# Kernel optimization log

Measured on AMD Instinct MI355X. Metric: run time of the kernel, lower is better.

The kernel has to match this reference:

```python
import jax, jax.numpy as jnp
import numpy as np


def _w1_1d(u, v):
    """POT-style 1D Wasserstein-1 between empirical dists of u and v (uniform weights).

    u, v: (N,) sample values. Follows ot.wasserstein_1d: sort samples, build
    cumulative weights, merge quantile levels, evaluate both quantile functions
    via searchsorted, and integrate |Q_u - Q_v| dq.
    """
    n = u.shape[0]
    u_s = jnp.sort(u)
    v_s = jnp.sort(v)
    # uniform weights -> identical cumulative weights for both distributions
    cw = jnp.cumsum(jnp.full((n,), 1.0 / n, dtype=u.dtype))
    qs = jnp.sort(jnp.concatenate([cw, cw]))  # (2N,) merged quantile levels
    idx = jnp.clip(jnp.searchsorted(cw, qs), 0, n - 1)  # quantile-function lookup
    uq = u_s[idx]
    vq = v_s[idx]
    delta = jnp.diff(qs, prepend=jnp.zeros((1,), dtype=u.dtype))  # dq segments
    return jnp.sum(delta * jnp.abs(uq - vq))


def setup_inputs() -> dict:
    key = jax.random.key(0)
    k1, k2 = jax.random.split(key)
    B, N = 4096, 4096
    return {
        "spectra_predict": jax.random.uniform(k1, (B, N), dtype=jnp.float32),
        "spectra_true": jax.random.uniform(k2, (B, N), dtype=jnp.float32),
    }


def reference(spectra_predict, spectra_true):
    # Original: wasserstein_1d(pred.T, true.T) batches over columns (= rows of
    # the untransposed [B, N] tensors), then mean over the batch.
    losses = jax.vmap(_w1_1d)(spectra_predict, spectra_true)  # (B,)
    return jnp.mean(losses)
```

## Files before the change

### kernel.cpp

```cpp
#include <hip/hip_runtime.h>


constexpr int N_ELEM  = 4096;
constexpr int V       = 32;
constexpr int THREADS = 256;

__device__ __forceinline__ float ce2(float x, float o, bool keep_min) {
    return ((o < x) != keep_min) ? x : o;
}

template<int S>
__device__ __forceinline__ void reg_merge(float r[V]) {
    #pragma unroll
    for (int k = 0; k < V; ++k) {
        if ((k & (S >> 1)) == 0) {
            const int j = k ^ (S - 1);
            const float a = r[k], b = r[j];
            r[k] = fminf(a, b);
            r[j] = fmaxf(a, b);
        }
    }
    #pragma unroll
    for (int s = S >> 2; s >= 1; s >>= 1) {
        #pragma unroll
        for (int k = 0; k < V; ++k) {
            if ((k & s) == 0) {
                const float a = r[k], b = r[k + s];
                r[k]     = fminf(a, b);
                r[k + s] = fmaxf(a, b);
            }
        }
    }
}

__device__ __forceinline__ void reg_tail_asc(float r[V]) {
    #pragma unroll
    for (int s = 16; s >= 1; s >>= 1) {
        #pragma unroll
        for (int k = 0; k < V; ++k) {
            if ((k & s) == 0) {
                const float a = r[k], b = r[k + s];
                r[k]     = fminf(a, b);
                r[k + s] = fmaxf(a, b);
            }
        }
    }
}

template<int CTRL>
__device__ __forceinline__ float dpp_x(float x) {
    return __int_as_float(__builtin_amdgcn_mov_dpp(__float_as_int(x), CTRL, 0xF, 0xF, true));
}
__device__ __forceinline__ float bperm_x(int pa, float x) {
    return __int_as_float(__builtin_amdgcn_ds_bpermute(pa, __float_as_int(x)));
}

template<int M>
__device__ __forceinline__ void xor_pass(float ru[V], float rv[V], int lane) {
    const bool keep_min = (lane & M) == 0;
    if constexpr (M == 1 || M == 2 || M == 8) {
        constexpr int ctrl = (M == 1) ? 0xB1 : (M == 2) ? 0x4E : 0x128;
        #pragma unroll
        for (int k = 0; k < V; ++k) {
            ru[k] = ce2(ru[k], dpp_x<ctrl>(ru[k]), keep_min);
            rv[k] = ce2(rv[k], dpp_x<ctrl>(rv[k]), keep_min);
        }
    } else {
        const int pa = (lane ^ M) << 2;
        float tu[16], tv[16];
        #pragma unroll
        for (int k = 0; k < 16; ++k) tu[k] = bperm_x(pa, ru[k]);
        #pragma unroll
        for (int k = 0; k < 16; ++k) tv[k] = bperm_x(pa, rv[k]);
        #pragma unroll
        for (int k = 0; k < 16; ++k) ru[k] = ce2(ru[k], tu[k], keep_min);
        #pragma unroll
        for (int k = 0; k < 16; ++k) tu[k] = bperm_x(pa, ru[16 + k]);
        #pragma unroll
        for (int k = 0; k < 16; ++k) rv[k] = ce2(rv[k], tv[k], keep_min);
        #pragma unroll
        for (int k = 0; k < 16; ++k) tv[k] = bperm_x(pa, rv[16 + k]);
        #pragma unroll
        for (int k = 0; k < 16; ++k) ru[16 + k] = ce2(ru[16 + k], tu[k], keep_min);
        #pragma unroll
        for (int k = 0; k < 16; ++k) rv[16 + k] = ce2(rv[16 + k], tv[k], keep_min);
    }
}

template<int MMAX>
__device__ __forceinline__ void cross_descend(float ru[V], float rv[V], int lane) {
    if constexpr (MMAX >= 32) xor_pass<32>(ru, rv, lane);
    if constexpr (MMAX >= 16) xor_pass<16>(ru, rv, lane);
    if constexpr (MMAX >= 8)  xor_pass<8>(ru, rv, lane);
    if constexpr (MMAX >= 4)  xor_pass<4>(ru, rv, lane);
    if constexpr (MMAX >= 2)  xor_pass<2>(ru, rv, lane);
    if constexpr (MMAX >= 1)  xor_pass<1>(ru, rv, lane);
    reg_tail_asc(ru);
    reg_tail_asc(rv);
}

template<int X>
static constexpr int mirror_dpp_ctrl() {
    return X == 1 ? 0xB1 : X == 3 ? 0x1B : X == 7 ? 0x141 : X == 15 ? 0x140 : -1;
}

template<int X>
__device__ __forceinline__ void mirror_pass(float ru[V], float rv[V], int lane) {
    const bool keep_min = (lane & ((X + 1) >> 1)) == 0;
    constexpr int ctrl = mirror_dpp_ctrl<X>();
    if constexpr (ctrl != -1) {
        #pragma unroll
        for (int k = 0; k < V / 2; ++k) {
            const int j = V - 1 - k;
            const float ua = dpp_x<ctrl>(ru[j]);
            const float ub = dpp_x<ctrl>(ru[k]);
            ru[k] = ce2(ru[k], ua, keep_min);
            ru[j] = ce2(ru[j], ub, keep_min);
            const float va = dpp_x<ctrl>(rv[j]);
            const float vb = dpp_x<ctrl>(rv[k]);
            rv[k] = ce2(rv[k], va, keep_min);
            rv[j] = ce2(rv[j], vb, keep_min);
        }
    } else {
        const int pa = (lane ^ X) << 2;
        #pragma unroll
        for (int k = 0; k < V / 2; ++k) {
            const int j = V - 1 - k;
            const float ua = bperm_x(pa, ru[j]);
            const float ub = bperm_x(pa, ru[k]);
            ru[k] = ce2(ru[k], ua, keep_min);
            ru[j] = ce2(ru[j], ub, keep_min);
            const float va = bperm_x(pa, rv[j]);
            const float vb = bperm_x(pa, rv[k]);
            rv[k] = ce2(rv[k], va, keep_min);
            rv[j] = ce2(rv[j], vb, keep_min);
        }
    }
}

template<int S>
__device__ __forceinline__ void stage_m(float ru[V], float rv[V], int lane) {
    mirror_pass<(S >> 5) - 1>(ru, rv, lane);
    cross_descend<(S >> 7)>(ru, rv, lane);
}

__global__ __launch_bounds__(THREADS, 4) void w1_rows_kernel(
    const float* __restrict__ pred,
    const float* __restrict__ tru,
    float* __restrict__ out,
    float scale)
{
    __shared__ float xbuf[2 * 128 * 33];
    __shared__ float wsum[THREADS / 64];

    const int tid  = threadIdx.x;
    const int t    = tid & 127;
    const int lane = tid & 63;
    const int row  = blockIdx.x * 2 + (tid >> 7);
    const size_t base = (size_t)row * N_ELEM + (size_t)t * V;

    float ru[V], rv[V];
    {
        const float4* u4 = (const float4*)(pred + base);
        const float4* v4 = (const float4*)(tru  + base);
        #pragma unroll
        for (int c = 0; c < V / 4; ++c) {
            float4 a = u4[c], b = v4[c];
            ru[4*c+0] = a.x; ru[4*c+1] = a.y; ru[4*c+2] = a.z; ru[4*c+3] = a.w;
            rv[4*c+0] = b.x; rv[4*c+1] = b.y; rv[4*c+2] = b.z; rv[4*c+3] = b.w;
        }
    }

    reg_merge<2>(ru);  reg_merge<2>(rv);
    reg_merge<4>(ru);  reg_merge<4>(rv);
    reg_merge<8>(ru);  reg_merge<8>(rv);
    reg_merge<16>(ru); reg_merge<16>(rv);
    reg_merge<32>(ru); reg_merge<32>(rv);

    stage_m<64>(ru, rv, lane);
    stage_m<128>(ru, rv, lane);
    stage_m<256>(ru, rv, lane);
    stage_m<512>(ru, rv, lane);
    stage_m<1024>(ru, rv, lane);
    stage_m<2048>(ru, rv, lane);

    {
        const bool is_upper = (t & 64) != 0;
        const int  slot_row = (tid >> 7) * 64;
        const int  my_u = (slot_row + lane) * 33;
        const int  my_v = 4224 + my_u;
        const int  pa_u = (slot_row + (63 - lane)) * 33;
        const int  pa_v = 4224 + pa_u;

        if (is_upper) {
            #pragma unroll
            for (int k = 0; k < V; ++k) xbuf[my_u + k] = ru[k];
            #pragma unroll
            for (int k = 0; k < V; ++k) xbuf[my_v + k] = rv[k];
        }
        __syncthreads();
        if (!is_upper) {
            #pragma unroll
            for (int k = 0; k < V; ++k) {
                const int  e = V - 1 - k;
                const float ou = xbuf[pa_u + e];
                const float ov = xbuf[pa_v + e];
                const float mu = fmaxf(ru[k], ou);
                const float mv = fmaxf(rv[k], ov);
                ru[k] = fminf(ru[k], ou);
                rv[k] = fminf(rv[k], ov);
                xbuf[pa_u + e] = mu;
                xbuf[pa_v + e] = mv;
            }
        }
        __syncthreads();
        if (is_upper) {
            #pragma unroll
            for (int k = 0; k < V; ++k) ru[k] = xbuf[my_u + k];
            #pragma unroll
            for (int k = 0; k < V; ++k) rv[k] = xbuf[my_v + k];
        }

        cross_descend<32>(ru, rv, lane);
    }

    float part = 0.f;
    #pragma unroll
    for (int k = 0; k < V; ++k) part += fabsf(ru[k] - rv[k]);

    #pragma unroll
    for (int off = 32; off > 0; off >>= 1)
        part += __shfl_down(part, off, 64);

    const int wid = tid >> 6;
    if (lane == 0) wsum[wid] = part;
    __syncthreads();
    if (tid == 0) {
        float tot = wsum[0] + wsum[1] + wsum[2] + wsum[3];
        atomicAdd(out, tot * scale);
    }
}

extern "C" void kernel_launch(void* const* d_in, const int* in_sizes, int n_in,
                              void* d_out, int out_size, void* d_ws, size_t ws_size,
                              hipStream_t stream)
{
    (void)n_in; (void)out_size; (void)d_ws; (void)ws_size;

    const float* pred = (const float*)d_in[0];
    const float* tru  = (const float*)d_in[1];
    float* out = (float*)d_out;

    const int B = in_sizes[0] / N_ELEM;

    hipMemsetAsync(out, 0, sizeof(float), stream);

    const float scale = 1.0f / ((float)N_ELEM * (float)B);
    w1_rows_kernel<<<B / 2, THREADS, 0, stream>>>(pred, tru, out, scale);
}
```

Measured before the change: 240.8 us.

## Split pred and true sorting across separate thread groups with 512-thread blocks

```diff
diff --git a/kernel.cpp b/kernel.cpp
--- a/kernel.cpp
+++ b/kernel.cpp
@@ -3,7 +3,7 @@
 
 constexpr int N_ELEM  = 4096;
 constexpr int V       = 32;
-constexpr int THREADS = 256;
+constexpr int THREADS = 512;
 
 __device__ __forceinline__ float ce2(float x, float o, bool keep_min) {
     return ((o < x) != keep_min) ? x : o;
@@ -56,47 +56,38 @@
 }
 
 template<int M>
-__device__ __forceinline__ void xor_pass(float ru[V], float rv[V], int lane) {
+__device__ __forceinline__ void xor_pass1(float r[V], int lane) {
     const bool keep_min = (lane & M) == 0;
     if constexpr (M == 1 || M == 2 || M == 8) {
         constexpr int ctrl = (M == 1) ? 0xB1 : (M == 2) ? 0x4E : 0x128;
         #pragma unroll
-        for (int k = 0; k < V; ++k) {
-            ru[k] = ce2(ru[k], dpp_x<ctrl>(ru[k]), keep_min);
-            rv[k] = ce2(rv[k], dpp_x<ctrl>(rv[k]), keep_min);
-        }
+        for (int k = 0; k < V; ++k)
+            r[k] = ce2(r[k], dpp_x<ctrl>(r[k]), keep_min);
     } else {
         const int pa = (lane ^ M) << 2;
-        float tu[16], tv[16];
-        #pragma unroll
-        for (int k = 0; k < 16; ++k) tu[k] = bperm_x(pa, ru[k]);
-        #pragma unroll
-        for (int k = 0; k < 16; ++k) tv[k] = bperm_x(pa, rv[k]);
-        #pragma unroll
-        for (int k = 0; k < 16; ++k) ru[k] = ce2(ru[k], tu[k], keep_min);
-        #pragma unroll
-        for (int k = 0; k < 16; ++k) tu[k] = bperm_x(pa, ru[16 + k]);
-        #pragma unroll
-        for (int k = 0; k < 16; ++k) rv[k] = ce2(rv[k], tv[k], keep_min);
-        #pragma unroll
-        for (int k = 0; k < 16; ++k) tv[k] = bperm_x(pa, rv[16 + k]);
-        #pragma unroll
-        for (int k = 0; k < 16; ++k) ru[16 + k] = ce2(ru[16 + k], tu[k], keep_min);
-        #pragma unroll
-        for (int k = 0; k < 16; ++k) rv[16 + k] = ce2(rv[16 + k], tv[k], keep_min);
+        float tt[16];
+        #pragma unroll
+        for (int k = 0; k < 16; ++k) tt[k] = bperm_x(pa, r[k]);
+        #pragma unroll
+        for (int k = 0; k < 16; ++k) {
+            r[k] = ce2(r[k], tt[k], keep_min);
+            tt[k] = bperm_x(pa, r[16 + k]);
+        }
+        #pragma unroll
+        for (int k = 0; k < 16; ++k)
+            r[16 + k] = ce2(r[16 + k], tt[k], keep_min);
     }
 }
 
 template<int MMAX>
-__device__ __forceinline__ void cross_descend(float ru[V], float rv[V], int lane) {
-    if constexpr (MMAX >= 32) xor_pass<32>(ru, rv, lane);
-    if constexpr (MMAX >= 16) xor_pass<16>(ru, rv, lane);
-    if constexpr (MMAX >= 8)  xor_pass<8>(ru, rv, lane);
-    if constexpr (MMAX >= 4)  xor_pass<4>(ru, rv, lane);
-    if constexpr (MMAX >= 2)  xor_pass<2>(ru, rv, lane);
-    if constexpr (MMAX >= 1)  xor_pass<1>(ru, rv, lane);
-    reg_tail_asc(ru);
-    reg_tail_asc(rv);
+__device__ __forceinline__ void cross_descend1(float r[V], int lane) {
+    if constexpr (MMAX >= 32) xor_pass1<32>(r, lane);
+    if constexpr (MMAX >= 16) xor_pass1<16>(r, lane);
+    if constexpr (MMAX >= 8)  xor_pass1<8>(r, lane);
+    if constexpr (MMAX >= 4)  xor_pass1<4>(r, lane);
+    if constexpr (MMAX >= 2)  xor_pass1<2>(r, lane);
+    if constexpr (MMAX >= 1)  xor_pass1<1>(r, lane);
+    reg_tail_asc(r);
 }
 
 template<int X>
@@ -105,128 +96,121 @@
 }
 
 template<int X>
-__device__ __forceinline__ void mirror_pass(float ru[V], float rv[V], int lane) {
+__device__ __forceinline__ void mirror_pass1(float r[V], int lane) {
     const bool keep_min = (lane & ((X + 1) >> 1)) == 0;
     constexpr int ctrl = mirror_dpp_ctrl<X>();
     if constexpr (ctrl != -1) {
         #pragma unroll
         for (int k = 0; k < V / 2; ++k) {
             const int j = V - 1 - k;
-            const float ua = dpp_x<ctrl>(ru[j]);
-            const float ub = dpp_x<ctrl>(ru[k]);
-            ru[k] = ce2(ru[k], ua, keep_min);
-            ru[j] = ce2(ru[j], ub, keep_min);
-            const float va = dpp_x<ctrl>(rv[j]);
-            const float vb = dpp_x<ctrl>(rv[k]);
-            rv[k] = ce2(rv[k], va, keep_min);
-            rv[j] = ce2(rv[j], vb, keep_min);
+            const float a = dpp_x<ctrl>(r[j]);
+            const float b = dpp_x<ctrl>(r[k]);
+            r[k] = ce2(r[k], a, keep_min);
+            r[j] = ce2(r[j], b, keep_min);
         }
     } else {
         const int pa = (lane ^ X) << 2;
         #pragma unroll
         for (int k = 0; k < V / 2; ++k) {
             const int j = V - 1 - k;
-            const float ua = bperm_x(pa, ru[j]);
-            const float ub = bperm_x(pa, ru[k]);
-            ru[k] = ce2(ru[k], ua, keep_min);
-            ru[j] = ce2(ru[j], ub, keep_min);
-            const float va = bperm_x(pa, rv[j]);
-            const float vb = bperm_x(pa, rv[k]);
-            rv[k] = ce2(rv[k], va, keep_min);
-            rv[j] = ce2(rv[j], vb, keep_min);
+            const float a = bperm_x(pa, r[j]);
+            const float b = bperm_x(pa, r[k]);
+            r[k] = ce2(r[k], a, keep_min);
+            r[j] = ce2(r[j], b, keep_min);
         }
     }
 }
 
 template<int S>
-__device__ __forceinline__ void stage_m(float ru[V], float rv[V], int lane) {
-    mirror_pass<(S >> 5) - 1>(ru, rv, lane);
-    cross_descend<(S >> 7)>(ru, rv, lane);
-}
-
-__global__ __launch_bounds__(THREADS, 4) void w1_rows_kernel(
+__device__ __forceinline__ void stage_m1(float r[V], int lane) {
+    mirror_pass1<(S >> 5) - 1>(r, lane);
+    cross_descend1<(S >> 7)>(r, lane);
+}
+
+__global__ __launch_bounds__(THREADS, 8) void w1_rows_kernel(
     const float* __restrict__ pred,
     const float* __restrict__ tru,
     float* __restrict__ out,
     float scale)
 {
-    __shared__ float xbuf[2 * 128 * 33];
+    __shared__ float xbuf[8448];
     __shared__ float wsum[THREADS / 64];
 
     const int tid  = threadIdx.x;
     const int t    = tid & 127;
     const int lane = tid & 63;
-    const int row  = blockIdx.x * 2 + (tid >> 7);
+    const int grp  = tid >> 7;
+    const int isv  = grp & 1;
+    const int row  = blockIdx.x * 2 + (tid >> 8);
+    const float* src = isv ? tru : pred;
     const size_t base = (size_t)row * N_ELEM + (size_t)t * V;
 
-    float ru[V], rv[V];
+    float r[V];
     {
-        const float4* u4 = (const float4*)(pred + base);
-        const float4* v4 = (const float4*)(tru  + base);
+        const float4* s4 = (const float4*)(src + base);
         #pragma unroll
         for (int c = 0; c < V / 4; ++c) {
-            float4 a = u4[c], b = v4[c];
-            ru[4*c+0] = a.x; ru[4*c+1] = a.y; ru[4*c+2] = a.z; ru[4*c+3] = a.w;
-            rv[4*c+0] = b.x; rv[4*c+1] = b.y; rv[4*c+2] = b.z; rv[4*c+3] = b.w;
-        }
-    }
-
-    reg_merge<2>(ru);  reg_merge<2>(rv);
-    reg_merge<4>(ru);  reg_merge<4>(rv);
-    reg_merge<8>(ru);  reg_merge<8>(rv);
-    reg_merge<16>(ru); reg_merge<16>(rv);
-    reg_merge<32>(ru); reg_merge<32>(rv);
-
-    stage_m<64>(ru, rv, lane);
-    stage_m<128>(ru, rv, lane);
-    stage_m<256>(ru, rv, lane);
-    stage_m<512>(ru, rv, lane);
-    stage_m<1024>(ru, rv, lane);
-    stage_m<2048>(ru, rv, lane);
+            float4 a = s4[c];
+            r[4*c+0] = a.x; r[4*c+1] = a.y; r[4*c+2] = a.z; r[4*c+3] = a.w;
+        }
+    }
+
+    reg_merge<2>(r);
+    reg_merge<4>(r);
+    reg_merge<8>(r);
+    reg_merge<16>(r);
+    reg_merge<32>(r);
+
+    stage_m1<64>(r, lane);
+    stage_m1<128>(r, lane);
+    stage_m1<256>(r, lane);
+    stage_m1<512>(r, lane);
+    stage_m1<1024>(r, lane);
+    stage_m1<2048>(r, lane);
 
     {
         const bool is_upper = (t & 64) != 0;
-        const int  slot_row = (tid >> 7) * 64;
-        const int  my_u = (slot_row + lane) * 33;
-        const int  my_v = 4224 + my_u;
-        const int  pa_u = (slot_row + (63 - lane)) * 33;
-        const int  pa_v = 4224 + pa_u;
+        const int  rb = grp * 2112;
+        const int  my = rb + lane * 33;
+        const int  pa = rb + (63 - lane) * 33;
 
         if (is_upper) {
             #pragma unroll
-            for (int k = 0; k < V; ++k) xbuf[my_u + k] = ru[k];
-            #pragma unroll
-            for (int k = 0; k < V; ++k) xbuf[my_v + k] = rv[k];
+            for (int k = 0; k < V; ++k) xbuf[my + k] = r[k];
         }
         __syncthreads();
         if (!is_upper) {
             #pragma unroll
             for (int k = 0; k < V; ++k) {
                 const int  e = V - 1 - k;
-                const float ou = xbuf[pa_u + e];
-                const float ov = xbuf[pa_v + e];
-                const float mu = fmaxf(ru[k], ou);
-                const float mv = fmaxf(rv[k], ov);
-                ru[k] = fminf(ru[k], ou);
-                rv[k] = fminf(rv[k], ov);
-                xbuf[pa_u + e] = mu;
-                xbuf[pa_v + e] = mv;
+                const float o  = xbuf[pa + e];
+                const float mx = fmaxf(r[k], o);
+                r[k] = fminf(r[k], o);
+                xbuf[pa + e] = mx;
             }
         }
         __syncthreads();
         if (is_upper) {
             #pragma unroll
-            for (int k = 0; k < V; ++k) ru[k] = xbuf[my_u + k];
-            #pragma unroll
-            for (int k = 0; k < V; ++k) rv[k] = xbuf[my_v + k];
-        }
-
-        cross_descend<32>(ru, rv, lane);
-    }
+            for (int k = 0; k < V; ++k) r[k] = xbuf[my + k];
+        }
+
+        cross_descend1<32>(r, lane);
+    }
+
+    __syncthreads();
+    const int pb = (tid >> 8) * 4224 + t * 33;
+    if (!isv) {
+        #pragma unroll
+        for (int k = 0; k < V; ++k) xbuf[pb + k] = r[k];
+    }
+    __syncthreads();
 
     float part = 0.f;
-    #pragma unroll
-    for (int k = 0; k < V; ++k) part += fabsf(ru[k] - rv[k]);
+    if (isv) {
+        #pragma unroll
+        for (int k = 0; k < V; ++k) part += fabsf(xbuf[pb + k] - r[k]);
+    }
 
     #pragma unroll
     for (int off = 32; off > 0; off >>= 1)
@@ -236,7 +220,9 @@
     if (lane == 0) wsum[wid] = part;
     __syncthreads();
     if (tid == 0) {
-        float tot = wsum[0] + wsum[1] + wsum[2] + wsum[3];
+        float tot = wsum[0];
+        #pragma unroll
+        for (int w = 1; w < THREADS / 64; ++w) tot += wsum[w];
         atomicAdd(out, tot * scale);
     }
 }
```

Measured after the change: 220.6 us. 1.09x faster.
